# Kernel tuning notes

Measured on AMD Instinct MI355X. Metric: run time of the kernel, lower is better.

The kernel has to match this reference:

```python
import jax, jax.numpy as jnp
import numpy as np

M = 4096   # out_features
N = 4096   # in_features
K_NNZ = 204  # nnz per row -> keep_ratio ~ 0.05
T = 8192   # tokens (batch*seq)


def setup_inputs() -> dict:
    key = jax.random.key(0)
    k1, k2, k3, k4 = jax.random.split(key, 4)
    # CSR structure: K_NNZ unique sorted columns per row (constant index buffers)
    rng = np.random.default_rng(0)
    cols = np.argsort(rng.random((M, N)), axis=1)[:, :K_NNZ]
    cols = np.sort(cols, axis=1).astype(np.int32)
    col_idx = jnp.asarray(cols.reshape(-1))                      # [nnz]
    row_ids = jnp.asarray(np.repeat(np.arange(M, dtype=np.int32), K_NNZ))  # [nnz]
    x = jax.random.normal(k1, (T, N), dtype=jnp.float32)
    dense_weight = jax.random.normal(k2, (M, N), dtype=jnp.float32) * 0.02
    bias = jax.random.normal(k3, (M,), dtype=jnp.float32) * 0.02
    sparse_values = jax.random.normal(k4, (M * K_NNZ,), dtype=jnp.float32) * 0.02
    return {"x": x, "dense_weight": dense_weight, "bias": bias,
            "sparse_values": sparse_values, "row_ids": row_ids, "col_idx": col_idx}


def reference(x, dense_weight, bias, sparse_values, row_ids, col_idx):
    # sp_add: scatter CSR values into the frozen dense weight (W = W_dense + W_sparse)
    W = dense_weight.at[row_ids, col_idx].add(sparse_values)     # [M, N]
    # sp_mm hot path: y = x @ W^T + b
    return jnp.dot(x, W.T) + bias                                # [T, M]
```

## Files before the change

### kernel.cpp

```cpp
#include <hip/hip_runtime.h>


typedef __attribute__((ext_vector_type(8))) __bf16 bf16x8;
typedef __attribute__((ext_vector_type(4))) float f32x4;
typedef __attribute__((ext_vector_type(8))) unsigned short u16x8;

#define BARRIER()   asm volatile("s_barrier" ::: "memory")
#define WAITVM0()   asm volatile("s_waitcnt vmcnt(0)" ::: "memory")
#define SCHED0()    __builtin_amdgcn_sched_barrier(0)

__device__ __forceinline__ unsigned short f2bf(float f) {
  unsigned int u = __builtin_bit_cast(unsigned int, f);
  u += 0x7FFFu + ((u >> 16) & 1u);
  return (unsigned short)(u >> 16);
}

__global__ __launch_bounds__(256) void cvt_f32_bf16(
    const float* __restrict__ s, unsigned short* __restrict__ d, long n8) {
  long i = (long)blockIdx.x * blockDim.x + threadIdx.x;
  const long stride = (long)gridDim.x * blockDim.x;
  for (; i < n8; i += stride) {
    const float4* sp = (const float4*)(s + i * 8);
    float4 a = sp[0];
    float4 b = sp[1];
    u16x8 o;
    o[0] = f2bf(a.x); o[1] = f2bf(a.y); o[2] = f2bf(a.z); o[3] = f2bf(a.w);
    o[4] = f2bf(b.x); o[5] = f2bf(b.y); o[6] = f2bf(b.z); o[7] = f2bf(b.w);
    *(u16x8*)(d + i * 8) = o;
  }
}

__global__ __launch_bounds__(256) void sparse_scatter(
    const float* __restrict__ dense, const float* __restrict__ vals,
    const int* __restrict__ rows, const int* __restrict__ cols,
    unsigned short* __restrict__ Wb, int nnz, int K) {
  int i = blockIdx.x * blockDim.x + threadIdx.x;
  if (i < nnz) {
    size_t off = (size_t)rows[i] * (size_t)K + (size_t)cols[i];
    Wb[off] = f2bf(dense[off] + vals[i]);
  }
}

__global__ __launch_bounds__(256, 1) void gemm4w(
    const unsigned short* __restrict__ A,
    const unsigned short* __restrict__ B,
    const float* __restrict__ bias,
    float* __restrict__ C,
    int Tm, int Mn, int K) {
  extern __shared__ __align__(16) char smem[];

  const int tid  = threadIdx.x;
  const int lane = tid & 63;
  const int wid  = tid >> 6;
  const int wm = (wid >> 1) * 128;
  const int wn = (wid & 1) * 128;

  const int nwg = gridDim.x;
  int bid = blockIdx.x;
  if ((nwg & 7) == 0) bid = (bid & 7) * (nwg >> 3) + (bid >> 3);
  const int ntn = Mn >> 8;
  const int bm0 = (bid / ntn) << 8;
  const int bn0 = (bid % ntn) << 8;

  const int NT = K >> 6;

  const int sr  = tid >> 3;
  const int gq8 = ((tid & 7) ^ (sr & 7)) * 8;
  const unsigned short* Asrc = A + (size_t)(bm0 + sr) * K + gq8;
  const unsigned short* Bsrc = B + (size_t)(bn0 + sr) * K + gq8;
  const size_t r32 = (size_t)32 * K;
  const int ldst = tid * 16;

#define STAGE8(SRC, LDSB, KOFF) do {                                             \
    _Pragma("unroll")                                                            \
    for (int c = 0; c < 8; ++c)                                                  \
      __builtin_amdgcn_global_load_lds(                                          \
        (const __attribute__((address_space(1))) void*)((SRC) + (size_t)c * r32 + (KOFF)), \
        (__attribute__((address_space(3))) void*)(smem + (LDSB) + c * 4096 + ldst), \
        16, 0, 0);                                                               \
  } while (0)

  const int fr = lane & 15, cq = lane >> 4;
  const int f7 = fr & 7;
  const int q0 = ((cq ^ f7) << 4);
  const int q1 = (((4 + cq) ^ f7) << 4);
  const int arow = (wm + fr) * 128;
  const int brow = (wn + fr) * 128;

  f32x4 acc[8][8] = {};
  bf16x8 a0[8], a1[8], b0[8], b1[8];

  STAGE8(Asrc, 0, 0);
  STAGE8(Bsrc, 32768, 0);
  WAITVM0();
  BARRIER();

#pragma unroll 2
  for (int t = 0; t < NT; ++t) {
    const char* Ab = smem + (t & 1) * 65536;
    const char* Bb = Ab + 32768;
    const int nbase = ((t & 1) ^ 1) * 65536;
    const int kn = (t + 1) * 64;
    const bool st = (t + 1 < NT);

#pragma unroll
    for (int m = 0; m < 8; ++m)
      a0[m] = *(const bf16x8*)(Ab + arow + m * 2048 + q0);
#pragma unroll
    for (int n = 0; n < 8; ++n)
      b0[n] = *(const bf16x8*)(Bb + brow + n * 2048 + q0);
    SCHED0();

    if (st) STAGE8(Asrc, nbase, kn);
    SCHED0();

#pragma unroll
    for (int m = 0; m < 8; ++m)
      a1[m] = *(const bf16x8*)(Ab + arow + m * 2048 + q1);
#pragma unroll
    for (int n = 0; n < 8; ++n)
      b1[n] = *(const bf16x8*)(Bb + brow + n * 2048 + q1);
    SCHED0();

    if (st) STAGE8(Bsrc, nbase + 32768, kn);
    SCHED0();

#pragma unroll
    for (int m = 0; m < 8; ++m)
#pragma unroll
      for (int n = 0; n < 8; ++n)
        acc[m][n] = __builtin_amdgcn_mfma_f32_16x16x32_bf16(a0[m], b0[n], acc[m][n], 0, 0, 0);
    SCHED0();

#pragma unroll
    for (int m = 0; m < 8; ++m)
#pragma unroll
      for (int n = 0; n < 8; ++n)
        acc[m][n] = __builtin_amdgcn_mfma_f32_16x16x32_bf16(a1[m], b1[n], acc[m][n], 0, 0, 0);

    WAITVM0();
    BARRIER();
  }
#undef STAGE8

  const int c4 = cq * 4;
#pragma unroll
  for (int n = 0; n < 8; ++n) {
    const int col = bn0 + wn + n * 16 + fr;
    const float bv = bias[col];
#pragma unroll
    for (int m = 0; m < 8; ++m) {
      const size_t rowb = (size_t)(bm0 + wm + m * 16 + c4);
#pragma unroll
      for (int q = 0; q < 4; ++q)
        C[(rowb + q) * (size_t)Mn + col] = acc[m][n][q] + bv;
    }
  }
}

extern "C" void kernel_launch(void* const* d_in, const int* in_sizes, int n_in,
                              void* d_out, int out_size, void* d_ws, size_t ws_size,
                              hipStream_t stream) {
  const float* x     = (const float*)d_in[0];
  const float* dw    = (const float*)d_in[1];
  const float* bias  = (const float*)d_in[2];
  const float* sv    = (const float*)d_in[3];
  const int*   rows  = (const int*)d_in[4];
  const int*   cols  = (const int*)d_in[5];
  float* out = (float*)d_out;

  const int  Mn = in_sizes[2];
  const long wElems = (long)in_sizes[1];
  const int  K  = (int)(wElems / Mn);
  const long xElems = (long)in_sizes[0];
  const int  Tm = (int)(xElems / K);
  const int  nnz = in_sizes[3];

  unsigned short* Wb = (unsigned short*)d_ws;
  unsigned short* Xb = Wb + wElems;

  cvt_f32_bf16<<<2048, 256, 0, stream>>>(dw, Wb, wElems / 8);
  sparse_scatter<<<(nnz + 255) / 256, 256, 0, stream>>>(dw, sv, rows, cols, Wb, nnz, K);
  cvt_f32_bf16<<<2048, 256, 0, stream>>>(x, Xb, xElems / 8);

  dim3 grid((Tm >> 8) * (Mn >> 8));
  gemm4w<<<grid, 256, 131072, stream>>>(Xb, Wb, bias, out, Tm, Mn, K);
}
```

Before: 307.3 us.

## Interleave MFMAs with LDS and global loads via sched_group_barrier; peel loop

Replaces the coarse sched_barrier phase separation with explicit sched_group_barrier patterns that interleave LDS reads, global-to-LDS stage loads and MFMA instructions. The K loop is unrolled by two with compile-time buffer offsets, and the last iteration is peeled so its stage, wait and branch disappear. The aim is to hide LDS and global load latency behind matrix math instead of issuing them in serialized phases. It relies on the compiler honoring the group masks, and register pressure and dependency stalls could change.

```diff
diff --git a/kernel.cpp b/kernel.cpp
--- a/kernel.cpp
+++ b/kernel.cpp
@@ -7,7 +7,7 @@
 
 #define BARRIER()   asm volatile("s_barrier" ::: "memory")
 #define WAITVM0()   asm volatile("s_waitcnt vmcnt(0)" ::: "memory")
-#define SCHED0()    __builtin_amdgcn_sched_barrier(0)
+#define SGB(m, n)   __builtin_amdgcn_sched_group_barrier((m), (n), 0)
 
 __device__ __forceinline__ unsigned short f2bf(float f) {
   unsigned int u = __builtin_bit_cast(unsigned int, f);
@@ -41,7 +41,7 @@
   }
 }
 
-__global__ __launch_bounds__(256, 1) void gemm4w(
+__global__ __launch_bounds__(256, 1) void gemm4wi(
     const unsigned short* __restrict__ A,
     const unsigned short* __restrict__ B,
     const float* __restrict__ bias,
@@ -95,52 +95,58 @@
   WAITVM0();
   BARRIER();
 
-#pragma unroll 2
-  for (int t = 0; t < NT; ++t) {
-    const char* Ab = smem + (t & 1) * 65536;
-    const char* Bb = Ab + 32768;
-    const int nbase = ((t & 1) ^ 1) * 65536;
-    const int kn = (t + 1) * 64;
-    const bool st = (t + 1 < NT);
+#define BODY(T_, RB_, SB_, ST_) do {                                             \
+    const char* Ab = smem + (RB_);                                               \
+    const char* Bb = smem + (RB_) + 32768;                                       \
+    const int kn = ((T_) + 1) << 6;                                              \
+    _Pragma("unroll")                                                            \
+    for (int m = 0; m < 8; ++m)                                                  \
+      a0[m] = *(const bf16x8*)(Ab + arow + m * 2048 + q0);                       \
+    _Pragma("unroll")                                                            \
+    for (int n = 0; n < 8; ++n)                                                  \
+      b0[n] = *(const bf16x8*)(Bb + brow + n * 2048 + q0);                       \
+    _Pragma("unroll")                                                            \
+    for (int m = 0; m < 8; ++m)                                                  \
+      a1[m] = *(const bf16x8*)(Ab + arow + m * 2048 + q1);                       \
+    _Pragma("unroll")                                                            \
+    for (int n = 0; n < 8; ++n)                                                  \
+      b1[n] = *(const bf16x8*)(Bb + brow + n * 2048 + q1);                       \
+    if (ST_) { STAGE8(Asrc, (SB_), kn); STAGE8(Bsrc, (SB_) + 32768, kn); }       \
+    _Pragma("unroll")                                                            \
+    for (int m = 0; m < 8; ++m)                                                  \
+      _Pragma("unroll")                                                          \
+      for (int n = 0; n < 8; ++n)                                                \
+        acc[m][n] = __builtin_amdgcn_mfma_f32_16x16x32_bf16(a0[m], b0[n], acc[m][n], 0, 0, 0); \
+    _Pragma("unroll")                                                            \
+    for (int m = 0; m < 8; ++m)                                                  \
+      _Pragma("unroll")                                                          \
+      for (int n = 0; n < 8; ++n)                                                \
+        acc[m][n] = __builtin_amdgcn_mfma_f32_16x16x32_bf16(a1[m], b1[n], acc[m][n], 0, 0, 0); \
+          \
+                                         \
+    SGB(0x100, 16);                                                              \
+    _Pragma("unroll")                                                            \
+    for (int g = 0; g < 16; ++g) { SGB(0x8, 4); SGB(0x100, 1); }                 \
+    if (ST_) {                                                                   \
+      _Pragma("unroll")                                                          \
+      for (int g = 0; g < 8; ++g) { SGB(0x8, 4); SGB(0x10, 1); }                 \
+      SGB(0x8, 32);                                                              \
+    } else {                                                                     \
+      SGB(0x8, 64);                                                              \
+    }                                                                            \
+    if (ST_) { WAITVM0(); }                                                      \
+    BARRIER();                                                                   \
+  } while (0)
 
-#pragma unroll
-    for (int m = 0; m < 8; ++m)
-      a0[m] = *(const bf16x8*)(Ab + arow + m * 2048 + q0);
-#pragma unroll
-    for (int n = 0; n < 8; ++n)
-      b0[n] = *(const bf16x8*)(Bb + brow + n * 2048 + q0);
-    SCHED0();
-
-    if (st) STAGE8(Asrc, nbase, kn);
-    SCHED0();
-
-#pragma unroll
-    for (int m = 0; m < 8; ++m)
-      a1[m] = *(const bf16x8*)(Ab + arow + m * 2048 + q1);
-#pragma unroll
-    for (int n = 0; n < 8; ++n)
-      b1[n] = *(const bf16x8*)(Bb + brow + n * 2048 + q1);
-    SCHED0();
-
-    if (st) STAGE8(Bsrc, nbase + 32768, kn);
-    SCHED0();
-
-#pragma unroll
-    for (int m = 0; m < 8; ++m)
-#pragma unroll
-      for (int n = 0; n < 8; ++n)
-        acc[m][n] = __builtin_amdgcn_mfma_f32_16x16x32_bf16(a0[m], b0[n], acc[m][n], 0, 0, 0);
-    SCHED0();
-
-#pragma unroll
-    for (int m = 0; m < 8; ++m)
-#pragma unroll
-      for (int n = 0; n < 8; ++n)
-        acc[m][n] = __builtin_amdgcn_mfma_f32_16x16x32_bf16(a1[m], b1[n], acc[m][n], 0, 0, 0);
-
-    WAITVM0();
-    BARRIER();
+  const int NPAIR = (NT >> 1) - 1;
+  for (int j = 0; j < NPAIR; ++j) {
+    const int t = 2 * j;
+    BODY(t,     0,     65536, 1);
+    BODY(t + 1, 65536, 0,     1);
   }
+  BODY(NT - 2, 0,     65536, 1);
+  BODY(NT - 1, 65536, 0,     0);
+#undef BODY
 #undef STAGE8
 
   const int c4 = cq * 4;
@@ -184,5 +190,5 @@
   cvt_f32_bf16<<<2048, 256, 0, stream>>>(x, Xb, xElems / 8);
 
   dim3 grid((Tm >> 8) * (Mn >> 8));
-  gemm4w<<<grid, 256, 131072, stream>>>(Xb, Wb, bias, out, Tm, Mn, K);
+  gemm4wi<<<grid, 256, 131072, stream>>>(Xb, Wb, bias, out, Tm, Mn, K);
 }
```

Result: slower. 383.0 us (+24.6%).

## Restructure GEMM to 8 waves with quadrant-pipelined LDS reads and MFMA

Applied to the files above, without the earlier changes.

Moves the bf16 GEMM from 4 waves per block (128x128 each) to 8 waves (128x64 each), halving per-wave accumulator registers. The main loop is split into four MFMA quadrants, with LDS fragment reads interleaved between them under explicit lgkmcnt waits. It also raises MFMA priority with s_setprio and issues next-next-tile global-to-LDS loads right after the barrier. This aims to hide LDS latency and improve overlap, at the cost of more waves sharing LDS bandwidth and more intricate synchronisation.

```diff
diff --git a/kernel.cpp b/kernel.cpp
--- a/kernel.cpp
+++ b/kernel.cpp
@@ -6,6 +6,7 @@
 typedef __attribute__((ext_vector_type(8))) unsigned short u16x8;
 
 #define BARRIER()   asm volatile("s_barrier" ::: "memory")
+#define WAITLGKM(n) asm volatile("s_waitcnt lgkmcnt(" #n ")" ::: "memory")
 #define WAITVM0()   asm volatile("s_waitcnt vmcnt(0)" ::: "memory")
 #define SCHED0()    __builtin_amdgcn_sched_barrier(0)
 
@@ -41,7 +42,7 @@
   }
 }
 
-__global__ __launch_bounds__(256, 1) void gemm4w(
+__global__ __launch_bounds__(512, 2) void gemm14(
     const unsigned short* __restrict__ A,
     const unsigned short* __restrict__ B,
     const float* __restrict__ bias,
@@ -52,8 +53,8 @@
   const int tid  = threadIdx.x;
   const int lane = tid & 63;
   const int wid  = tid >> 6;
-  const int wm = (wid >> 1) * 128;
-  const int wn = (wid & 1) * 128;
+  const int wm = (wid >> 2) * 128;
+  const int wn = (wid & 3) * 64;
 
   const int nwg = gridDim.x;
   int bid = blockIdx.x;
@@ -68,16 +69,23 @@
   const int gq8 = ((tid & 7) ^ (sr & 7)) * 8;
   const unsigned short* Asrc = A + (size_t)(bm0 + sr) * K + gq8;
   const unsigned short* Bsrc = B + (size_t)(bn0 + sr) * K + gq8;
-  const size_t r32 = (size_t)32 * K;
+  const size_t r64 = (size_t)64 * K;
   const int ldst = tid * 16;
 
-#define STAGE8(SRC, LDSB, KOFF) do {                                             \
-    _Pragma("unroll")                                                            \
-    for (int c = 0; c < 8; ++c)                                                  \
-      __builtin_amdgcn_global_load_lds(                                          \
-        (const __attribute__((address_space(1))) void*)((SRC) + (size_t)c * r32 + (KOFF)), \
-        (__attribute__((address_space(3))) void*)(smem + (LDSB) + c * 4096 + ldst), \
-        16, 0, 0);                                                               \
+#define STAGEH(SRC, H, LDSB, KOFF) do {                                          \
+    __builtin_amdgcn_global_load_lds(                                            \
+      (const __attribute__((address_space(1))) void*)((SRC) + (size_t)(H)*2*r64 + (KOFF)), \
+      (__attribute__((address_space(3))) void*)(smem + (LDSB) + ldst), 16, 0, 0);\
+    __builtin_amdgcn_global_load_lds(                                            \
+      (const __attribute__((address_space(1))) void*)((SRC) + (size_t)(H)*2*r64 + r64 + (KOFF)), \
+      (__attribute__((address_space(3))) void*)(smem + (LDSB) + 8192 + ldst), 16, 0, 0); \
+  } while (0)
+
+#define STAGEALL(NB, KO) do {                                                    \
+    STAGEH(Asrc, 0, (NB), (KO));                                                 \
+    STAGEH(Asrc, 1, (NB) + 16384, (KO));                                         \
+    STAGEH(Bsrc, 0, (NB) + 32768, (KO));                                         \
+    STAGEH(Bsrc, 1, (NB) + 49152, (KO));                                         \
   } while (0)
 
   const int fr = lane & 15, cq = lane >> 4;
@@ -87,65 +95,104 @@
   const int arow = (wm + fr) * 128;
   const int brow = (wn + fr) * 128;
 
-  f32x4 acc[8][8] = {};
-  bf16x8 a0[8], a1[8], b0[8], b1[8];
-
-  STAGE8(Asrc, 0, 0);
-  STAGE8(Bsrc, 32768, 0);
+  f32x4 acc[8][4] = {};
+  bf16x8 Aq0[4], Aq1[4];
+  bf16x8 b1q0[2], b1q1[2], b2q0[2], b2q1[2];
+
+#define READ12(BUF) do {                                                         \
+    _Pragma("unroll")                                                            \
+    for (int m = 0; m < 4; ++m) {                                                \
+      Aq0[m] = *(const bf16x8*)((BUF) + arow + m * 2048 + q0);                   \
+      Aq1[m] = *(const bf16x8*)((BUF) + arow + m * 2048 + q1);                   \
+    }                                                                            \
+    _Pragma("unroll")                                                            \
+    for (int n = 0; n < 2; ++n) {                                                \
+      b1q0[n] = *(const bf16x8*)((BUF) + 32768 + brow + n * 2048 + q0);          \
+      b1q1[n] = *(const bf16x8*)((BUF) + 32768 + brow + n * 2048 + q1);          \
+    }                                                                            \
+  } while (0)
+
+#define READB23(BUF) do {                                                        \
+    _Pragma("unroll")                                                            \
+    for (int n = 0; n < 2; ++n) {                                                \
+      b2q0[n] = *(const bf16x8*)((BUF) + 32768 + brow + (n + 2) * 2048 + q0);    \
+      b2q1[n] = *(const bf16x8*)((BUF) + 32768 + brow + (n + 2) * 2048 + q1);    \
+    }                                                                            \
+  } while (0)
+
+#define READA47(BUF) do {                                                        \
+    _Pragma("unroll")                                                            \
+    for (int m = 0; m < 4; ++m) {                                                \
+      Aq0[m] = *(const bf16x8*)((BUF) + arow + (m + 4) * 2048 + q0);             \
+      Aq1[m] = *(const bf16x8*)((BUF) + arow + (m + 4) * 2048 + q1);             \
+    }                                                                            \
+  } while (0)
+
+#define QUAD(MB, NB, BQ0, BQ1) do {                                              \
+    __builtin_amdgcn_s_setprio(1);                                               \
+    _Pragma("unroll")                                                            \
+    for (int m = 0; m < 4; ++m)                                                  \
+      _Pragma("unroll")                                                          \
+      for (int n = 0; n < 2; ++n) {                                              \
+        acc[m+(MB)][n+(NB)] = __builtin_amdgcn_mfma_f32_16x16x32_bf16(           \
+            Aq0[m], BQ0[n], acc[m+(MB)][n+(NB)], 0, 0, 0);                       \
+        acc[m+(MB)][n+(NB)] = __builtin_amdgcn_mfma_f32_16x16x32_bf16(           \
+            Aq1[m], BQ1[n], acc[m+(MB)][n+(NB)], 0, 0, 0);                       \
+      }                                                                          \
+    __builtin_amdgcn_s_setprio(0);                                               \
+  } while (0)
+
+  STAGEALL(0, 0);
   WAITVM0();
   BARRIER();
-
-#pragma unroll 2
+  READ12(smem);
+  SCHED0();
+  if (NT > 1) STAGEALL(65536, 64);
+  SCHED0();
+
   for (int t = 0; t < NT; ++t) {
-    const char* Ab = smem + (t & 1) * 65536;
-    const char* Bb = Ab + 32768;
-    const int nbase = ((t & 1) ^ 1) * 65536;
-    const int kn = (t + 1) * 64;
-    const bool st = (t + 1 < NT);
-
-#pragma unroll
-    for (int m = 0; m < 8; ++m)
-      a0[m] = *(const bf16x8*)(Ab + arow + m * 2048 + q0);
-#pragma unroll
-    for (int n = 0; n < 8; ++n)
-      b0[n] = *(const bf16x8*)(Bb + brow + n * 2048 + q0);
-    SCHED0();
-
-    if (st) STAGE8(Asrc, nbase, kn);
-    SCHED0();
-
-#pragma unroll
-    for (int m = 0; m < 8; ++m)
-      a1[m] = *(const bf16x8*)(Ab + arow + m * 2048 + q1);
-#pragma unroll
-    for (int n = 0; n < 8; ++n)
-      b1[n] = *(const bf16x8*)(Bb + brow + n * 2048 + q1);
-    SCHED0();
-
-    if (st) STAGE8(Bsrc, nbase + 32768, kn);
-    SCHED0();
-
-#pragma unroll
-    for (int m = 0; m < 8; ++m)
-#pragma unroll
-      for (int n = 0; n < 8; ++n)
-        acc[m][n] = __builtin_amdgcn_mfma_f32_16x16x32_bf16(a0[m], b0[n], acc[m][n], 0, 0, 0);
-    SCHED0();
-
-#pragma unroll
-    for (int m = 0; m < 8; ++m)
-#pragma unroll
-      for (int n = 0; n < 8; ++n)
-        acc[m][n] = __builtin_amdgcn_mfma_f32_16x16x32_bf16(a1[m], b1[n], acc[m][n], 0, 0, 0);
-
+    const char* buf = smem + (t & 1) * 65536;
+
+    READB23(buf);
+    SCHED0();
+    WAITLGKM(4);
+    SCHED0();
+    QUAD(0, 0, b1q0, b1q1);
+    SCHED0();
+
+    WAITLGKM(0);
+    SCHED0();
+    QUAD(0, 2, b2q0, b2q1);
+    SCHED0();
+    READA47(buf);
+    SCHED0();
+
+    WAITLGKM(0);
+    SCHED0();
+    QUAD(4, 0, b1q0, b1q1);
     WAITVM0();
     BARRIER();
-  }
-#undef STAGE8
+
+    QUAD(4, 2, b2q0, b2q1);
+    SCHED0();
+    if (t + 1 < NT) {
+      const char* nbuf = smem + ((t + 1) & 1) * 65536;
+      READ12(nbuf);
+      SCHED0();
+      if (t + 2 < NT) STAGEALL((t & 1) * 65536, (t + 2) * 64);
+      SCHED0();
+    }
+  }
+#undef QUAD
+#undef READA47
+#undef READB23
+#undef READ12
+#undef STAGEALL
+#undef STAGEH
 
   const int c4 = cq * 4;
 #pragma unroll
-  for (int n = 0; n < 8; ++n) {
+  for (int n = 0; n < 4; ++n) {
     const int col = bn0 + wn + n * 16 + fr;
     const float bv = bias[col];
 #pragma unroll
@@ -184,5 +231,5 @@
   cvt_f32_bf16<<<2048, 256, 0, stream>>>(x, Xb, xElems / 8);
 
   dim3 grid((Tm >> 8) * (Mn >> 8));
-  gemm4w<<<grid, 256, 131072, stream>>>(Xb, Wb, bias, out, Tm, Mn, K);
-}
+  gemm14<<<grid, 512, 131072, stream>>>(Xb, Wb, bias, out, Tm, Mn, K);
+}
```

Result: no change. 302.5 us (-1.6%).

## Shrink GEMM tile to 128x256 with triple-buffered K=32 LDS ring

Applied to the files above, without the earlier changes.

Reworks the bf16 GEMM from a 256x256 tile with a double-buffered K=64 LDS stage (128 KB) to a 128x256 tile with a three-deep K=32 ring (72 KB). This allows two workgroups per CU and a prefetch distance of two stages, using partial vmcnt waits and s_setprio around the MFMA block. The aim is better latency hiding and occupancy. In exchange the tile has lower arithmetic intensity and needs a barrier on every shorter iteration.

```diff
diff --git a/kernel.cpp b/kernel.cpp
--- a/kernel.cpp
+++ b/kernel.cpp
@@ -6,7 +6,8 @@
 typedef __attribute__((ext_vector_type(8))) unsigned short u16x8;
 
 #define BARRIER()   asm volatile("s_barrier" ::: "memory")
-#define WAITVM0()   asm volatile("s_waitcnt vmcnt(0)" ::: "memory")
+#define WAITLGKM0() asm volatile("s_waitcnt lgkmcnt(0)" ::: "memory")
+#define WAITVM(n)   asm volatile("s_waitcnt vmcnt(" #n ")" ::: "memory")
 #define SCHED0()    __builtin_amdgcn_sched_barrier(0)
 
 __device__ __forceinline__ unsigned short f2bf(float f) {
@@ -41,7 +42,7 @@
   }
 }
 
-__global__ __launch_bounds__(256, 1) void gemm4w(
+__global__ __launch_bounds__(256, 2) void gemm2b(
     const unsigned short* __restrict__ A,
     const unsigned short* __restrict__ B,
     const float* __restrict__ bias,
@@ -52,96 +53,82 @@
   const int tid  = threadIdx.x;
   const int lane = tid & 63;
   const int wid  = tid >> 6;
-  const int wm = (wid >> 1) * 128;
+  const int wm = (wid >> 1) * 64;
   const int wn = (wid & 1) * 128;
 
   const int nwg = gridDim.x;
   int bid = blockIdx.x;
   if ((nwg & 7) == 0) bid = (bid & 7) * (nwg >> 3) + (bid >> 3);
   const int ntn = Mn >> 8;
-  const int bm0 = (bid / ntn) << 8;
+  const int bm0 = (bid / ntn) << 7;
   const int bn0 = (bid % ntn) << 8;
 
-  const int NT = K >> 6;
+  const int NT = K >> 5;
 
-  const int sr  = tid >> 3;
-  const int gq8 = ((tid & 7) ^ (sr & 7)) * 8;
-  const unsigned short* Asrc = A + (size_t)(bm0 + sr) * K + gq8;
-  const unsigned short* Bsrc = B + (size_t)(bn0 + sr) * K + gq8;
-  const size_t r32 = (size_t)32 * K;
+  const int srow = tid >> 2;
+  const int sq8  = ((tid & 3) ^ ((tid >> 2) & 3) ^ ((tid >> 4) & 3)) * 8;
+  const unsigned short* Asrc = A + (size_t)(bm0 + srow) * K + sq8;
+  const unsigned short* Bsrc = B + (size_t)(bn0 + srow) * K + sq8;
+  const size_t r64 = (size_t)64 * K;
   const int ldst = tid * 16;
 
-#define STAGE8(SRC, LDSB, KOFF) do {                                             \
+#define STAGE(RING, KOFF) do {                                                   \
     _Pragma("unroll")                                                            \
-    for (int c = 0; c < 8; ++c)                                                  \
+    for (int c = 0; c < 2; ++c)                                                  \
       __builtin_amdgcn_global_load_lds(                                          \
-        (const __attribute__((address_space(1))) void*)((SRC) + (size_t)c * r32 + (KOFF)), \
-        (__attribute__((address_space(3))) void*)(smem + (LDSB) + c * 4096 + ldst), \
+        (const __attribute__((address_space(1))) void*)(Asrc + (size_t)c * r64 + (KOFF)), \
+        (__attribute__((address_space(3))) void*)(smem + (RING) + c * 4096 + ldst), \
+        16, 0, 0);                                                               \
+    _Pragma("unroll")                                                            \
+    for (int c = 0; c < 4; ++c)                                                  \
+      __builtin_amdgcn_global_load_lds(                                          \
+        (const __attribute__((address_space(1))) void*)(Bsrc + (size_t)c * r64 + (KOFF)), \
+        (__attribute__((address_space(3))) void*)(smem + (RING) + 8192 + c * 4096 + ldst), \
         16, 0, 0);                                                               \
   } while (0)
 
   const int fr = lane & 15, cq = lane >> 4;
-  const int f7 = fr & 7;
-  const int q0 = ((cq ^ f7) << 4);
-  const int q1 = (((4 + cq) ^ f7) << 4);
-  const int arow = (wm + fr) * 128;
-  const int brow = (wn + fr) * 128;
+  const int qoff = ((cq ^ (fr & 3) ^ ((fr >> 2) & 3)) << 4);
+  const int abase = (wm + fr) * 64 + qoff;
+  const int bbase = 8192 + (wn + fr) * 64 + qoff;
 
-  f32x4 acc[8][8] = {};
-  bf16x8 a0[8], a1[8], b0[8], b1[8];
+  f32x4 acc[4][8] = {};
+  bf16x8 a[4], b[8];
 
-  STAGE8(Asrc, 0, 0);
-  STAGE8(Bsrc, 32768, 0);
-  WAITVM0();
+  STAGE(0, 0);
+  STAGE(24576, 32);
+  WAITVM(6);
   BARRIER();
 
-#pragma unroll 2
+  int rr = 0;
   for (int t = 0; t < NT; ++t) {
-    const char* Ab = smem + (t & 1) * 65536;
-    const char* Bb = Ab + 32768;
-    const int nbase = ((t & 1) ^ 1) * 65536;
-    const int kn = (t + 1) * 64;
-    const bool st = (t + 1 < NT);
+    int sr_ = rr + 49152; if (sr_ >= 73728) sr_ -= 73728;
+    if (t + 2 < NT) STAGE(sr_, (t + 2) * 32);
 
+    const char* buf = smem + rr;
 #pragma unroll
-    for (int m = 0; m < 8; ++m)
-      a0[m] = *(const bf16x8*)(Ab + arow + m * 2048 + q0);
+    for (int m = 0; m < 4; ++m)
+      a[m] = *(const bf16x8*)(buf + abase + m * 1024);
 #pragma unroll
     for (int n = 0; n < 8; ++n)
-      b0[n] = *(const bf16x8*)(Bb + brow + n * 2048 + q0);
+      b[n] = *(const bf16x8*)(buf + bbase + n * 1024);
+
+    if (t + 2 < NT)      { WAITVM(6); }
+    else if (t + 1 < NT) { WAITVM(0); }
+    WAITLGKM0();
     SCHED0();
-
-    if (st) STAGE8(Asrc, nbase, kn);
-    SCHED0();
-
+    __builtin_amdgcn_s_setprio(1);
 #pragma unroll
-    for (int m = 0; m < 8; ++m)
-      a1[m] = *(const bf16x8*)(Ab + arow + m * 2048 + q1);
-#pragma unroll
-    for (int n = 0; n < 8; ++n)
-      b1[n] = *(const bf16x8*)(Bb + brow + n * 2048 + q1);
-    SCHED0();
-
-    if (st) STAGE8(Bsrc, nbase + 32768, kn);
-    SCHED0();
-
-#pragma unroll
-    for (int m = 0; m < 8; ++m)
+    for (int m = 0; m < 4; ++m)
 #pragma unroll
       for (int n = 0; n < 8; ++n)
-        acc[m][n] = __builtin_amdgcn_mfma_f32_16x16x32_bf16(a0[m], b0[n], acc[m][n], 0, 0, 0);
-    SCHED0();
+        acc[m][n] = __builtin_amdgcn_mfma_f32_16x16x32_bf16(a[m], b[n], acc[m][n], 0, 0, 0);
+    __builtin_amdgcn_s_setprio(0);
+    BARRIER();
 
-#pragma unroll
-    for (int m = 0; m < 8; ++m)
-#pragma unroll
-      for (int n = 0; n < 8; ++n)
-        acc[m][n] = __builtin_amdgcn_mfma_f32_16x16x32_bf16(a1[m], b1[n], acc[m][n], 0, 0, 0);
-
-    WAITVM0();
-    BARRIER();
+    rr += 24576; if (rr >= 73728) rr = 0;
   }
-#undef STAGE8
+#undef STAGE
 
   const int c4 = cq * 4;
 #pragma unroll
@@ -149,7 +136,7 @@
     const int col = bn0 + wn + n * 16 + fr;
     const float bv = bias[col];
 #pragma unroll
-    for (int m = 0; m < 8; ++m) {
+    for (int m = 0; m < 4; ++m) {
       const size_t rowb = (size_t)(bm0 + wm + m * 16 + c4);
 #pragma unroll
       for (int q = 0; q < 4; ++q)
@@ -183,6 +170,6 @@
   sparse_scatter<<<(nnz + 255) / 256, 256, 0, stream>>>(dw, sv, rows, cols, Wb, nnz, K);
   cvt_f32_bf16<<<2048, 256, 0, stream>>>(x, Xb, xElems / 8);
 
-  dim3 grid((Tm >> 8) * (Mn >> 8));
-  gemm4w<<<grid, 256, 131072, stream>>>(Xb, Wb, bias, out, Tm, Mn, K);
+  dim3 grid((Tm >> 7) * (Mn >> 8));
+  gemm2b<<<grid, 256, 73728, stream>>>(Xb, Wb, bias, out, Tm, Mn, K);
 }
```

Result: slower. 346.2 us (+12.7%).
